# Kernel optimization log

Hardware: AMD Instinct MI355X
Metric: run time of the kernel (lower is better)

Reference implementation:

```python
import jax, jax.numpy as jnp
import numpy as np

NEG_SLOPE = 0.2  # PyG GATConv default negative_slope
EPS = 1e-16      # PyG softmax denominator epsilon


def setup_inputs() -> dict:
    key = jax.random.key(0)
    N, C, H, E = 50000, 64, 12, 400000
    k = jax.random.split(key, 5)
    x = jax.random.normal(k[0], (N, C), dtype=jnp.float32)
    edge_index = jax.random.randint(k[1], (2, E), 0, N, dtype=jnp.int32)
    W = jax.random.normal(k[2], (C, H * C), dtype=jnp.float32) * (1.0 / np.sqrt(C))
    att_src = jax.random.normal(k[3], (H, C), dtype=jnp.float32) * 0.1
    att_dst = jax.random.normal(k[4], (H, C), dtype=jnp.float32) * 0.1
    bias = jnp.zeros((C,), dtype=jnp.float32)
    return {"x": x, "edge_index": edge_index, "W": W,
            "att_src": att_src, "att_dst": att_dst, "bias": bias}


def reference(x, edge_index, W, att_src, att_dst, bias):
    N, C = x.shape
    H = att_src.shape[0]
    # GATConv default add_self_loops=True
    loops = jnp.arange(N, dtype=edge_index.dtype)
    src = jnp.concatenate([edge_index[0], loops])  # message source j
    dst = jnp.concatenate([edge_index[1], loops])  # message target i

    h = (x @ W).reshape(N, H, C)                   # [N,H,C] projected features
    a_src = jnp.einsum('nhc,hc->nh', h, att_src)   # [N,H]
    a_dst = jnp.einsum('nhc,hc->nh', h, att_dst)   # [N,H]

    alpha = jax.nn.leaky_relu(a_src[src] + a_dst[dst], NEG_SLOPE)  # [E',H]
    # segment softmax over destination neighborhoods
    m = jax.ops.segment_max(alpha, dst, num_segments=N)
    alpha = jnp.exp(alpha - m[dst])
    denom = jax.ops.segment_sum(alpha, dst, num_segments=N)
    alpha = alpha / (denom[dst] + EPS)

    msg = h[src] * alpha[:, :, None]               # [E',H,C]
    out = jax.ops.segment_sum(msg, dst, num_segments=N)  # [N,H,C]
    y = out.mean(axis=1) + bias                    # concat=False -> head mean
    return jax.nn.relu(x + y)
```

## Files before the change

### kernel.cpp

```cpp
#include <hip/hip_runtime.h>
#include <hip/hip_bf16.h>


typedef __bf16 bf16x8 __attribute__((ext_vector_type(8)));
typedef float  f32x4  __attribute__((ext_vector_type(4)));
typedef float  f32x2  __attribute__((ext_vector_type(2)));

#define HEADS 12
#define CH 64
#define HC 768
#define CAP 64
#define ACOLS 24
#define ZSTRIDE 776

__device__ inline float readlane_f(float v, int lane) {
    return __builtin_bit_cast(float,
        __builtin_amdgcn_readlane(__builtin_bit_cast(int, v), lane));
}

__global__ __launch_bounds__(256) void k_pre(
    const float* __restrict__ W,
    const float* __restrict__ att_src, const float* __restrict__ att_dst,
    int* __restrict__ cnt, __bf16* __restrict__ Wt2, __bf16* __restrict__ Vt,
    int N) {
    const int nb_z = (N + 255) >> 8;
    const int nb_w = (CH * HC) >> 8;
    int b = blockIdx.x, tid = threadIdx.x;
    if (b < nb_z) {
        int i = b * 256 + tid;
        if (i < N) cnt[i] = 0;
        return;
    }
    b -= nb_z;
    if (b < nb_w) {
        int t = b * 256 + tid;
        int c = t / HC, kk = t % HC;
        int k = kk & 63;
        Wt2[t] = (__bf16)W[(size_t)k * HC + (kk - k) + c];
        return;
    }
    b -= nb_w;
    if (b >= 2 * HEADS) {
        if (tid < CH) Vt[b * CH + tid] = (__bf16)0.f;
        return;
    }
    const float* att = (b < HEADS) ? att_src + b * CH
                                   : att_dst + (b - HEADS) * CH;
    int k = tid >> 2, cq = tid & 3;
    const float* wr = W + (size_t)k * HC + (b % HEADS) * CH + cq * 16;
    float s = 0.f;
#pragma unroll
    for (int j = 0; j < 16; ++j) s += wr[j] * att[cq * 16 + j];
    s += __shfl_xor(s, 1, 64);
    s += __shfl_xor(s, 2, 64);
    if (cq == 0) Vt[b * CH + k] = (__bf16)s;
}

__global__ __launch_bounds__(256) void k_main(
    const float* __restrict__ x, const int* __restrict__ ei,
    const __bf16* __restrict__ Vt,
    int* __restrict__ cnt, int* __restrict__ adj,
    __bf16* __restrict__ xb, float* __restrict__ a_all, int N, int E) {
    const int EP = E + N;
    const int nb_build = (EP + 255) >> 8;
    int b = blockIdx.x, tid = threadIdx.x;

    if (b < nb_build) {
        int e = b * 256 + tid;
        if (e < EP) {
            int d, s;
            if (e < E) { d = ei[E + e]; s = ei[e]; }
            else       { d = e - E;     s = d; }
            int pos = atomicAdd(&cnt[d], 1);
            if (pos < CAP) adj[d * CAP + pos] = s;
        }
        return;
    }
    b -= nb_build;
    int wave = tid >> 6, lane = tid & 63;
    int m = lane & 15, quad = lane >> 4;
    int m0 = b * 64 + wave * 16;
    int row = m0 + m;
    int rc = row < N ? row : N - 1;
    const float* xa = x + (size_t)rc * CH + quad * 8;
    f32x4 v0 = *(const f32x4*)xa;
    f32x4 v1 = *(const f32x4*)(xa + 4);
    f32x4 v2 = *(const f32x4*)(xa + 32);
    f32x4 v3 = *(const f32x4*)(xa + 36);
    bf16x8 a0, a1;
#pragma unroll
    for (int j = 0; j < 4; ++j) {
        a0[j] = (__bf16)v0[j]; a0[4 + j] = (__bf16)v1[j];
        a1[j] = (__bf16)v2[j]; a1[4 + j] = (__bf16)v3[j];
    }
    if (row < N) {
        *(bf16x8*)(xb + (size_t)row * CH + quad * 8) = a0;
        *(bf16x8*)(xb + (size_t)row * CH + quad * 8 + 32) = a1;
    }
#pragma unroll
    for (int t = 0; t < 2; ++t) {
        const __bf16* bp = Vt + (size_t)(t * 16 + m) * CH + quad * 8;
        bf16x8 b0 = *(const bf16x8*)bp;
        bf16x8 b1 = *(const bf16x8*)(bp + 32);
        f32x4 acc = {0.f, 0.f, 0.f, 0.f};
        acc = __builtin_amdgcn_mfma_f32_16x16x32_bf16(a0, b0, acc, 0, 0, 0);
        acc = __builtin_amdgcn_mfma_f32_16x16x32_bf16(a1, b1, acc, 0, 0, 0);
        int col = t * 16 + m;
        if (col < ACOLS) {
#pragma unroll
            for (int r = 0; r < 4; ++r) {
                int rr = m0 + quad * 4 + r;
                if (rr < N) a_all[(size_t)rr * ACOLS + col] = acc[r];
            }
        }
    }
}

__global__ __launch_bounds__(256) void k_fused(
    const int* __restrict__ cnt, const int* __restrict__ adj,
    const float* __restrict__ a_all,
    const __bf16* __restrict__ xb, const __bf16* __restrict__ Wt2,
    const float* __restrict__ x, const float* __restrict__ bias,
    float* __restrict__ out, int N) {
    __shared__ __bf16 zt[16 * ZSTRIDE];
    int wave = threadIdx.x >> 6, lane = threadIdx.x & 63;
    int base = blockIdx.x * 16;

    int degj[4], slj[4];
#pragma unroll
    for (int j = 0; j < 4; ++j) {
        int d = base + wave * 4 + j;
        int dg = cnt[d];
        degj[j] = dg < CAP ? dg : CAP;
        int sraw = (lane < 32) ? adj[d * CAP + lane] : 0;
        slj[j] = sraw < 0 ? 0 : (sraw >= N ? N - 1 : sraw);
    }
#pragma unroll
    for (int j = 0; j < 4; ++j) {
        if (degj[j] > 32 && lane >= 32) {
            int sraw = adj[(base + wave * 4 + j) * CAP + lane];
            slj[j] = sraw < 0 ? 0 : (sraw >= N ? N - 1 : sraw);
        }
    }

    f32x4 asb[2][3], adb[2][3];
    {
        const f32x4* pa = (const f32x4*)(a_all + (size_t)(base + wave * 4) * ACOLS + HEADS);
        adb[0][0] = pa[0]; adb[0][1] = pa[1]; adb[0][2] = pa[2];
        const f32x4* ps = (const f32x4*)(a_all + (size_t)slj[0] * ACOLS);
        asb[0][0] = ps[0]; asb[0][1] = ps[1]; asb[0][2] = ps[2];
    }

#pragma unroll
    for (int j = 0; j < 4; ++j) {
        int cur = j & 1, nxt = cur ^ 1;
        int row = wave * 4 + j;
        int deg = degj[j];
        int deg4 = (deg + 3) & ~3;
        int s_l = slj[j];

        float w[HEADS];
        {
            float pad = (lane < deg) ? 0.f : -1e30f;
#pragma unroll
            for (int g = 0; g < 3; ++g) {
#pragma unroll
                for (int u = 0; u < 4; ++u) {
                    float sc = asb[cur][g][u] + adb[cur][g][u];
                    sc = sc > 0.f ? sc : 0.2f * sc;
                    w[g * 4 + u] = __expf(sc + pad);
                }
            }
        }

        if (j < 3) {
            const f32x4* pa = (const f32x4*)(a_all + (size_t)(base + wave * 4 + j + 1) * ACOLS + HEADS);
            adb[nxt][0] = pa[0]; adb[nxt][1] = pa[1]; adb[nxt][2] = pa[2];
            const f32x4* ps = (const f32x4*)(a_all + (size_t)slj[j + 1] * ACOLS);
            asb[nxt][0] = ps[0]; asb[nxt][1] = ps[1]; asb[nxt][2] = ps[2];
        }

        f32x2 acc2[HEADS];
#pragma unroll
        for (int hh = 0; hh < HEADS; ++hh) acc2[hh] = (f32x2){0.f, 0.f};
        for (int i = 0; i < deg4; i += 4) {
            int s0 = __builtin_amdgcn_readlane(s_l, i);
            int s1 = __builtin_amdgcn_readlane(s_l, i + 1);
            int s2 = __builtin_amdgcn_readlane(s_l, i + 2);
            int s3 = __builtin_amdgcn_readlane(s_l, i + 3);
            f32x2 xv0 = {(float)xb[(size_t)s0 * CH + lane], 1.f};
            f32x2 xv1 = {(float)xb[(size_t)s1 * CH + lane], 1.f};
            f32x2 xv2 = {(float)xb[(size_t)s2 * CH + lane], 1.f};
            f32x2 xv3 = {(float)xb[(size_t)s3 * CH + lane], 1.f};
#pragma unroll
            for (int hh = 0; hh < HEADS; ++hh) {
                float w0 = readlane_f(w[hh], i);
                float w1 = readlane_f(w[hh], i + 1);
                float w2 = readlane_f(w[hh], i + 2);
                float w3 = readlane_f(w[hh], i + 3);
                acc2[hh] += (f32x2){w0, w0} * xv0;
                acc2[hh] += (f32x2){w1, w1} * xv1;
                acc2[hh] += (f32x2){w2, w2} * xv2;
                acc2[hh] += (f32x2){w3, w3} * xv3;
            }
        }
        __bf16* zr = zt + row * ZSTRIDE + lane;
#pragma unroll
        for (int hh = 0; hh < HEADS; ++hh)
            zr[hh * CH] = (__bf16)(acc2[hh].x * (1.0f / ((acc2[hh].y + 1e-16f) * HEADS)));
    }

    __syncthreads();

    {
        int m = lane & 15, quad = lane >> 4;
        int n0 = wave * 16;
        const __bf16* za = zt + m * ZSTRIDE + quad * 8;
        const __bf16* wb = Wt2 + (size_t)(n0 + m) * HC + quad * 8;
        f32x4 acc = {0.f, 0.f, 0.f, 0.f};
#pragma unroll
        for (int kc = 0; kc < HC; kc += 32) {
            bf16x8 a  = *(const bf16x8*)(za + kc);
            bf16x8 bf = *(const bf16x8*)(wb + kc);
            acc = __builtin_amdgcn_mfma_f32_16x16x32_bf16(a, bf, acc, 0, 0, 0);
        }
        int col = n0 + m;
        float bv = bias[col];
#pragma unroll
        for (int r = 0; r < 4; ++r) {
            int dd = base + quad * 4 + r;
            if (dd < N) {
                float o = x[(size_t)dd * CH + col] + acc[r] + bv;
                out[(size_t)dd * CH + col] = fmaxf(o, 0.f);
            }
        }
    }
}

extern "C" void kernel_launch(void* const* d_in, const int* in_sizes, int n_in,
                              void* d_out, int out_size, void* d_ws, size_t ws_size,
                              hipStream_t stream) {
    const float* x       = (const float*)d_in[0];
    const int*   ei      = (const int*)d_in[1];
    const float* W       = (const float*)d_in[2];
    const float* att_src = (const float*)d_in[3];
    const float* att_dst = (const float*)d_in[4];
    const float* bias    = (const float*)d_in[5];
    float* out = (float*)d_out;

    int N = in_sizes[0] / CH;
    int E = in_sizes[1] / 2;
    int EP = E + N;

    char* ws = (char*)d_ws;
    size_t off = 0;
    auto take = [&](size_t bytes) -> void* {
        void* p = ws + off;
        off = (off + bytes + 255) & ~(size_t)255;
        return p;
    };
    __bf16* xb    = (__bf16*)take((size_t)N * CH * sizeof(__bf16));
    __bf16* Wt2   = (__bf16*)take((size_t)CH * HC * sizeof(__bf16));
    __bf16* Vt    = (__bf16*)take((size_t)32 * CH * sizeof(__bf16));
    float*  a_all = (float*)take((size_t)N * ACOLS * sizeof(float));
    int*    adj   = (int*)take((size_t)N * CAP * sizeof(int));
    int*    cnt   = (int*)take((size_t)N * sizeof(int));

    const int nb_z     = (N + 255) / 256;
    const int nb_w     = (CH * HC) / 256;
    const int nb_build = (EP + 255) / 256;
    const int nb_ax    = (N + 63) / 64;

    k_pre<<<nb_z + nb_w + 32, 256, 0, stream>>>(W, att_src, att_dst, cnt, Wt2, Vt, N);
    k_main<<<nb_build + nb_ax, 256, 0, stream>>>(x, ei, Vt, cnt, adj, xb, a_all, N, E);
    k_fused<<<(N + 15) / 16, 256, 0, stream>>>(cnt, adj, a_all, xb, Wt2, x, bias, out, N);
}
```

Baseline: 179.9 us.

## Compute softmax denominators via wave shuffles and specialize edge aggregation by degree

The softmax denominator is now summed with cross-lane xor shuffles instead of being carried as a second component of every packed FMA. Edge aggregation uses fixed-size unrolled blocks of 8 or 16 edges with all gathers issued first, then a scalar tail loop for higher degrees. The double-buffered prefetch of attention scores across rows is removed, and scores are loaded just before use. The aim is to halve the FMA work and improve memory-level parallelism for typical low-degree nodes. In exchange, padded edges in the fixed blocks are wasted work, 72 shuffles are added per row, and load latency is now exposed.

```diff
diff --git a/kernel.cpp b/kernel.cpp
--- a/kernel.cpp
+++ b/kernel.cpp
@@ -4,7 +4,6 @@
 
 typedef __bf16 bf16x8 __attribute__((ext_vector_type(8)));
 typedef float  f32x4  __attribute__((ext_vector_type(4)));
-typedef float  f32x2  __attribute__((ext_vector_type(2)));
 
 #define HEADS 12
 #define CH 64
@@ -116,6 +115,24 @@
     }
 }
 
+template <int NE>
+__device__ __forceinline__ void agg_edges(int s_l, const float* w,
+                                          const __bf16* __restrict__ xb,
+                                          int lane, float* acc) {
+    float xv[NE];
+#pragma unroll
+    for (int e = 0; e < NE; ++e) {
+        int s = __builtin_amdgcn_readlane(s_l, e);
+        xv[e] = (float)xb[(size_t)s * CH + lane];
+    }
+#pragma unroll
+    for (int e = 0; e < NE; ++e) {
+#pragma unroll
+        for (int hh = 0; hh < HEADS; ++hh)
+            acc[hh] += readlane_f(w[hh], e) * xv[e];
+    }
+}
+
 __global__ __launch_bounds__(256) void k_fused(
     const int* __restrict__ cnt, const int* __restrict__ adj,
     const float* __restrict__ a_all,
@@ -143,71 +160,64 @@
         }
     }
 
-    f32x4 asb[2][3], adb[2][3];
-    {
-        const f32x4* pa = (const f32x4*)(a_all + (size_t)(base + wave * 4) * ACOLS + HEADS);
-        adb[0][0] = pa[0]; adb[0][1] = pa[1]; adb[0][2] = pa[2];
-        const f32x4* ps = (const f32x4*)(a_all + (size_t)slj[0] * ACOLS);
-        asb[0][0] = ps[0]; asb[0][1] = ps[1]; asb[0][2] = ps[2];
-    }
-
-#pragma unroll
-    for (int j = 0; j < 4; ++j) {
-        int cur = j & 1, nxt = cur ^ 1;
+    for (int j = 0; j < 4; ++j) {
         int row = wave * 4 + j;
+        int d = base + row;
         int deg = degj[j];
-        int deg4 = (deg + 3) & ~3;
         int s_l = slj[j];
 
         float w[HEADS];
         {
+            const f32x4* pa = (const f32x4*)(a_all + (size_t)d * ACOLS + HEADS);
+            f32x4 d0 = pa[0], d1 = pa[1], d2 = pa[2];
+            const f32x4* ps = (const f32x4*)(a_all + (size_t)s_l * ACOLS);
+            f32x4 s0 = ps[0], s1 = ps[1], s2 = ps[2];
             float pad = (lane < deg) ? 0.f : -1e30f;
 #pragma unroll
-            for (int g = 0; g < 3; ++g) {
-#pragma unroll
-                for (int u = 0; u < 4; ++u) {
-                    float sc = asb[cur][g][u] + adb[cur][g][u];
-                    sc = sc > 0.f ? sc : 0.2f * sc;
-                    w[g * 4 + u] = __expf(sc + pad);
-                }
-            }
-        }
-
-        if (j < 3) {
-            const f32x4* pa = (const f32x4*)(a_all + (size_t)(base + wave * 4 + j + 1) * ACOLS + HEADS);
-            adb[nxt][0] = pa[0]; adb[nxt][1] = pa[1]; adb[nxt][2] = pa[2];
-            const f32x4* ps = (const f32x4*)(a_all + (size_t)slj[j + 1] * ACOLS);
-            asb[nxt][0] = ps[0]; asb[nxt][1] = ps[1]; asb[nxt][2] = ps[2];
-        }
-
-        f32x2 acc2[HEADS];
-#pragma unroll
-        for (int hh = 0; hh < HEADS; ++hh) acc2[hh] = (f32x2){0.f, 0.f};
-        for (int i = 0; i < deg4; i += 4) {
-            int s0 = __builtin_amdgcn_readlane(s_l, i);
-            int s1 = __builtin_amdgcn_readlane(s_l, i + 1);
-            int s2 = __builtin_amdgcn_readlane(s_l, i + 2);
-            int s3 = __builtin_amdgcn_readlane(s_l, i + 3);
-            f32x2 xv0 = {(float)xb[(size_t)s0 * CH + lane], 1.f};
-            f32x2 xv1 = {(float)xb[(size_t)s1 * CH + lane], 1.f};
-            f32x2 xv2 = {(float)xb[(size_t)s2 * CH + lane], 1.f};
-            f32x2 xv3 = {(float)xb[(size_t)s3 * CH + lane], 1.f};
-#pragma unroll
-            for (int hh = 0; hh < HEADS; ++hh) {
-                float w0 = readlane_f(w[hh], i);
-                float w1 = readlane_f(w[hh], i + 1);
-                float w2 = readlane_f(w[hh], i + 2);
-                float w3 = readlane_f(w[hh], i + 3);
-                acc2[hh] += (f32x2){w0, w0} * xv0;
-                acc2[hh] += (f32x2){w1, w1} * xv1;
-                acc2[hh] += (f32x2){w2, w2} * xv2;
-                acc2[hh] += (f32x2){w3, w3} * xv3;
-            }
-        }
+            for (int u = 0; u < 4; ++u) {
+                float sc;
+                sc = s0[u] + d0[u]; sc = sc > 0.f ? sc : 0.2f * sc;
+                w[u] = __expf(sc + pad);
+                sc = s1[u] + d1[u]; sc = sc > 0.f ? sc : 0.2f * sc;
+                w[4 + u] = __expf(sc + pad);
+                sc = s2[u] + d2[u]; sc = sc > 0.f ? sc : 0.2f * sc;
+                w[8 + u] = __expf(sc + pad);
+            }
+        }
+
+        float den[HEADS];
+#pragma unroll
+        for (int hh = 0; hh < HEADS; ++hh) {
+            float s = w[hh];
+            s += __shfl_xor(s, 1, 64);
+            s += __shfl_xor(s, 2, 64);
+            s += __shfl_xor(s, 4, 64);
+            s += __shfl_xor(s, 8, 64);
+            s += __shfl_xor(s, 16, 64);
+            s += __shfl_xor(s, 32, 64);
+            den[hh] = s;
+        }
+
+        float acc[HEADS];
+#pragma unroll
+        for (int hh = 0; hh < HEADS; ++hh) acc[hh] = 0.f;
+        if (deg <= 8) {
+            agg_edges<8>(s_l, w, xb, lane, acc);
+        } else {
+            agg_edges<16>(s_l, w, xb, lane, acc);
+            for (int i = 16; i < deg; ++i) {
+                int s = __builtin_amdgcn_readlane(s_l, i);
+                float xv = (float)xb[(size_t)s * CH + lane];
+#pragma unroll
+                for (int hh = 0; hh < HEADS; ++hh)
+                    acc[hh] += readlane_f(w[hh], i) * xv;
+            }
+        }
+
         __bf16* zr = zt + row * ZSTRIDE + lane;
 #pragma unroll
         for (int hh = 0; hh < HEADS; ++hh)
-            zr[hh * CH] = (__bf16)(acc2[hh].x * (1.0f / ((acc2[hh].y + 1e-16f) * HEADS)));
+            zr[hh * CH] = (__bf16)(acc[hh] * (1.0f / ((den[hh] + 1e-16f) * HEADS)));
     }
 
     __syncthreads();
```

Result: slower. 195.8 us (+8.8%).
